# Kernel optimization log

Hardware: AMD Instinct MI355X
Metric: run time of the kernel (lower is better)

Reference implementation:

```python
import jax, jax.numpy as jnp
import numpy as np

B, T, C, H = 512, 40, 512, 512


def _gru_dir(x, Wih, Whh, bih, bhh):
    """Single-direction PyTorch-convention GRU. x: [B,T,C] -> [B,T,H]."""
    Hh = Whh.shape[1]
    # precompute input projections for all timesteps: [B,T,3H]
    gx = jnp.einsum('btc,gc->btg', x, Wih) + bih

    def step(h, gxt):
        gh = h @ Whh.T + bhh  # [B,3H]
        r = jax.nn.sigmoid(gxt[:, :Hh] + gh[:, :Hh])
        z = jax.nn.sigmoid(gxt[:, Hh:2 * Hh] + gh[:, Hh:2 * Hh])
        n = jnp.tanh(gxt[:, 2 * Hh:] + r * gh[:, 2 * Hh:])
        h_new = (1.0 - z) * n + z * h
        return h_new, h_new

    h0 = jnp.zeros((x.shape[0], Hh), x.dtype)
    _, ys = jax.lax.scan(step, h0, jnp.swapaxes(gx, 0, 1))  # [T,B,H]
    return jnp.swapaxes(ys, 0, 1)


def setup_inputs() -> dict:
    key = jax.random.key(0)
    ks = jax.random.split(key, 10)
    s = 1.0 / np.sqrt(H)  # PyTorch default init scale
    lengths = jax.random.randint(ks[0], (B,), 5, T + 1)
    valid = jnp.arange(T)[None, :] < lengths[:, None]  # [B,T]
    ref_expr = jax.random.normal(ks[1], (B, T, C), jnp.float32) * valid[..., None]
    mk = lambda k, shape: jax.random.uniform(k, shape, jnp.float32, -s, s)
    return {
        'ref_expr': ref_expr,
        'Wih_f': mk(ks[2], (3 * H, C)), 'Whh_f': mk(ks[3], (3 * H, H)),
        'bih_f': mk(ks[4], (3 * H,)), 'bhh_f': mk(ks[5], (3 * H,)),
        'Wih_b': mk(ks[6], (3 * H, C)), 'Whh_b': mk(ks[7], (3 * H, H)),
        'bih_b': mk(ks[8], (3 * H,)), 'bhh_b': mk(ks[9], (3 * H,)),
    }


def reference(ref_expr, Wih_f, Whh_f, bih_f, bhh_f, Wih_b, Whh_b, bih_b, bhh_b):
    # padded positions are all-zero embedding vectors -> masked out
    valid = jnp.any(ref_expr != 0, axis=-1)  # [B,T], True = keep
    y_fwd = _gru_dir(ref_expr, Wih_f, Whh_f, bih_f, bhh_f)
    y_bwd = _gru_dir(ref_expr[:, ::-1], Wih_b, Whh_b, bih_b, bhh_b)[:, ::-1]
    y_word = jnp.concatenate([y_fwd, y_bwd], axis=-1)  # [B,T,2H]
    # masked max pooling over valid tokens (output_type='max')
    neg = jnp.finfo(y_word.dtype).min
    y = jnp.max(jnp.where(valid[..., None], y_word, neg), axis=1, keepdims=True)
    return y  # [B,1,2H]
```

## Files before the change

kernel.cpp:

```cpp
#include <hip/hip_runtime.h>
#include <hip/hip_bf16.h>
#include <float.h>

#define BB 512
#define TT 40
#define CC 512
#define HH 512

typedef short bf16x8 __attribute__((ext_vector_type(8)));
typedef float f32x4 __attribute__((ext_vector_type(4)));
typedef unsigned short ushortx8 __attribute__((ext_vector_type(8)));

#define LDSH 49152
#define LDSF 98304
#define LDSTOT 98320

__device__ __forceinline__ unsigned short f2bf(float f){
  union { float f; unsigned int i; } v; v.f = f;
  unsigned int r = v.i + 0x7fffu + ((v.i >> 16) & 1u);
  return (unsigned short)(r >> 16);
}

__device__ __forceinline__ bf16x8 load_sc0(const unsigned short* p){
  bf16x8 r;
  asm volatile("global_load_dwordx4 %0, %1, off sc0" : "=v"(r) : "v"(p));
  return r;
}
#define WAITV(N) do { asm volatile("s_waitcnt vmcnt(" #N ")" ::: "memory"); \
                      __builtin_amdgcn_sched_barrier(0); } while(0)

__device__ __forceinline__ void waitv_idx(int n){
  switch(n){
    case 0:  WAITV(0);  break;  case 1:  WAITV(1);  break;
    case 2:  WAITV(2);  break;  case 3:  WAITV(3);  break;
    case 4:  WAITV(4);  break;  case 5:  WAITV(5);  break;
    case 6:  WAITV(6);  break;  case 7:  WAITV(7);  break;
    case 8:  WAITV(8);  break;  case 9:  WAITV(9);  break;
    case 10: WAITV(10); break;  case 11: WAITV(11); break;
    case 12: WAITV(12); break;  case 13: WAITV(13); break;
    case 14: WAITV(14); break;  default: WAITV(15); break;
  }
}

__device__ __forceinline__ float fast_sigmoid(float x){
  return __builtin_amdgcn_rcpf(1.f + __expf(-x));
}
__device__ __forceinline__ float fast_tanh(float x){
  return 1.f - 2.f*__builtin_amdgcn_rcpf(__expf(2.f*x) + 1.f);
}

__global__ void prep_x_kernel(const float* __restrict__ x, unsigned short* __restrict__ xb,
                              float* __restrict__ maskT){
  int w = blockIdx.x*4 + (threadIdx.x>>6);
  int lane = threadIdx.x & 63;
  const float* src = x + (size_t)w*CC + lane*8;
  f32x4 a = *(const f32x4*)(src);
  f32x4 b = *(const f32x4*)(src+4);
  ushortx8 o;
  o[0]=f2bf(a[0]); o[1]=f2bf(a[1]); o[2]=f2bf(a[2]); o[3]=f2bf(a[3]);
  o[4]=f2bf(b[0]); o[5]=f2bf(b[1]); o[6]=f2bf(b[2]); o[7]=f2bf(b[3]);
  *(ushortx8*)(xb + (size_t)w*CC + lane*8) = o;
  bool nz = (a[0]!=0.f)||(a[1]!=0.f)||(a[2]!=0.f)||(a[3]!=0.f)||
            (b[0]!=0.f)||(b[1]!=0.f)||(b[2]!=0.f)||(b[3]!=0.f);
  unsigned long long bal = __ballot(nz);
  if (lane==0){
    int b_ = w / TT, t_ = w % TT;
    maskT[t_*BB + b_] = bal ? 1.0f : 0.0f;
  }
}

__global__ void cvt_kernel(const float* __restrict__ src, unsigned short* __restrict__ dst, int n8){
  int i = blockIdx.x*blockDim.x + threadIdx.x;
  if (i < n8){
    f32x4 a = *(const f32x4*)(src + i*8);
    f32x4 b = *(const f32x4*)(src + i*8 + 4);
    ushortx8 o;
    o[0]=f2bf(a[0]); o[1]=f2bf(a[1]); o[2]=f2bf(a[2]); o[3]=f2bf(a[3]);
    o[4]=f2bf(b[0]); o[5]=f2bf(b[1]); o[6]=f2bf(b[2]); o[7]=f2bf(b[3]);
    *(ushortx8*)(dst + i*8) = o;
  }
}

__global__ void init_h_kernel(unsigned short* __restrict__ hb, unsigned int* __restrict__ flags){
  int i = blockIdx.x*blockDim.x + threadIdx.x;
  hb[i] = 0;
  if (i < 256) flags[i] = 0u;
}

__global__ __launch_bounds__(512, 2) void gru_persist_kernel(
    const unsigned short* __restrict__ xb,
    const unsigned short* __restrict__ wihF, const unsigned short* __restrict__ whhF,
    const unsigned short* __restrict__ wihB, const unsigned short* __restrict__ whhB,
    const float* __restrict__ bihF, const float* __restrict__ bhhF,
    const float* __restrict__ bihB, const float* __restrict__ bhhB,
    const float* __restrict__ maskT,
    unsigned short* __restrict__ hb,
    float* __restrict__ out, unsigned int* __restrict__ flags)
{
  const int bid   = blockIdx.x;
  const int grp   = bid & 7;
  const int strip = bid >> 3;
  const int dir   = grp >> 2;
  const int bslab = grp & 3;
  const int b0 = bslab * 128;
  const int n0 = strip * 16;
  unsigned int* fl = flags + grp*32;

  const unsigned short* wih = dir ? wihB : wihF;
  const unsigned short* whh = dir ? whhB : whhF;
  const float* bih = dir ? bihB : bihF;
  const float* bhh = dir ? bhhB : bhhF;

  const int tid  = threadIdx.x;
  const int lane = tid & 63;
  const int lr   = lane & 15;
  const int lkg  = lane >> 4;
  const int wv   = tid >> 6;
  const int wrow = wv * 16;

  __shared__ __align__(16) char smem[LDSTOT];
  unsigned int* arrive = (unsigned int*)(smem + LDSF);

  for (int q = tid; q < 6144; q += 512) {
    const int p_  = q >= 3072;
    const int r_  = p_ ? (q - 3072) : q;
    const int row = r_ >> 6;
    const int kc  = (r_ & 63) * 8;
    const unsigned short* src =
        (p_ ? whh : wih) + ((size_t)((row>>4)*HH + n0 + (row&15)))*512 + kc;
    *(ushortx8*)(smem + p_*LDSH + row*1024 + ((kc*2) ^ ((row&15)<<4))) =
        *(const ushortx8*)src;
  }
  if (tid == 0) arrive[0] = 0u;
  __syncthreads();

  const int jj = n0 + lr;
  const float br  = bih[jj]        + bhh[jj];
  const float bz  = bih[HH + jj]   + bhh[HH + jj];
  const float bnx = bih[2*HH + jj];
  const float bnh = bhh[2*HH + jj];

  float omax[4], hreg[4];
  #pragma unroll
  for (int j=0; j<4; ++j){ omax[j] = -FLT_MAX; hreg[j] = 0.f; }

  const int swz = lr << 4;
  const char* wbx = smem + lr*1024;
  const char* wbh = smem + LDSH + lr*1024;

  for (int t = 0; t < TT; ++t) {
    const int tx = dir ? (TT-1-t) : t;
    const int bi = t & 1;
    const unsigned short* hbin = hb + (size_t)(dir*2 + bi)      * (BB*HH);
    unsigned short* hbout      = hb + (size_t)(dir*2 + (bi^1))  * (BB*HH);

    f32x4 ar = 0.f, az = 0.f, anx = 0.f, anh = 0.f;

    const unsigned short* xr0 = xb + ((size_t)(b0 + wrow + lr)*TT + tx)*CC;

    #pragma unroll
    for (int kk = 0; kk < 16; ++kk) {
      const int ko = kk*32 + lkg*8;
      bf16x8 a0 = *(const bf16x8*)(xr0 + ko);
      const int kbx = (ko*2) ^ swz;
      bf16x8 brf = *(const bf16x8*)(wbx +         kbx);
      bf16x8 bzf = *(const bf16x8*)(wbx + 16384 + kbx);
      bf16x8 bnf = *(const bf16x8*)(wbx + 32768 + kbx);
      ar  = __builtin_amdgcn_mfma_f32_16x16x32_bf16(a0, brf, ar,0,0,0);
      az  = __builtin_amdgcn_mfma_f32_16x16x32_bf16(a0, bzf, az,0,0,0);
      anx = __builtin_amdgcn_mfma_f32_16x16x32_bf16(a0, bnf, anx,0,0,0);
    }

    const f32x4 mk = *(const f32x4*)(maskT + tx*BB + b0 + wrow + lkg*4);

    if (t > 0) {
      const unsigned int tgt = (unsigned)t;
      unsigned int spin = 0;
      for (;;) {
        unsigned int v = tgt;
        if (lane < 32)
          v = __hip_atomic_load(&fl[lane], __ATOMIC_RELAXED, __HIP_MEMORY_SCOPE_AGENT);
        if (__ballot(v < tgt) == 0ull) break;
        if (++spin >= (1u<<22)) break;
        __builtin_amdgcn_s_sleep(1);
      }
    }

    WAITV(0);

    const unsigned short* hr0 = hbin + (size_t)(b0 + wrow + lr)*HH;
    bf16x8 ph[16];
    #pragma unroll
    for (int q = 0; q < 16; ++q)
      ph[q] = load_sc0(hr0 + q*32 + lkg*8);
    #pragma unroll
    for (int kk = 0; kk < 16; ++kk) {
      const int ko = kk*32 + lkg*8;
      const int kbx = (ko*2) ^ swz;
      bf16x8 brf = *(const bf16x8*)(wbh +         kbx);
      bf16x8 bzf = *(const bf16x8*)(wbh + 16384 + kbx);
      bf16x8 bnf = *(const bf16x8*)(wbh + 32768 + kbx);
      waitv_idx(15 - kk);
      bf16x8 c0 = ph[kk];
      ar  = __builtin_amdgcn_mfma_f32_16x16x32_bf16(c0, brf, ar,0,0,0);
      az  = __builtin_amdgcn_mfma_f32_16x16x32_bf16(c0, bzf, az,0,0,0);
      anh = __builtin_amdgcn_mfma_f32_16x16x32_bf16(c0, bnf, anh,0,0,0);
    }

    #pragma unroll
    for (int j=0; j<4; ++j){
      const int b = b0 + wrow + lkg*4 + j;
      const float rg = fast_sigmoid(ar[j] + br);
      const float zg = fast_sigmoid(az[j] + bz);
      const float ng = fast_tanh(anx[j] + bnx + rg*(anh[j] + bnh));
      const float hn = (1.f - zg)*ng + zg*hreg[j];
      hreg[j] = hn;
      hbout[(size_t)b*HH + jj] = f2bf(hn);
      const float cand = (mk[j] != 0.f) ? hn : -FLT_MAX;
      omax[j] = fmaxf(omax[j], cand);
    }

    if (t < TT-1) {
      WAITV(0);
      if (lane == 0) {
        unsigned int prev =
            __hip_atomic_fetch_add(arrive, 1u, __ATOMIC_ACQ_REL, __HIP_MEMORY_SCOPE_WORKGROUP);
        if (prev + 1u == 8u*(unsigned)(t+1))
          __hip_atomic_store(&fl[strip], (unsigned)(t+1),
                             __ATOMIC_RELAXED, __HIP_MEMORY_SCOPE_AGENT);
      }
    }
  }

  #pragma unroll
  for (int j=0; j<4; ++j){
    const int b = b0 + wrow + lkg*4 + j;
    out[(size_t)b*(2*HH) + dir*HH + jj] = omax[j];
  }
}

extern "C" void kernel_launch(void* const* d_in, const int* in_sizes, int n_in,
                              void* d_out, int out_size, void* d_ws, size_t ws_size,
                              hipStream_t stream) {
  const float* x    = (const float*)d_in[0];
  const float* WihF = (const float*)d_in[1];
  const float* WhhF = (const float*)d_in[2];
  const float* bihF = (const float*)d_in[3];
  const float* bhhF = (const float*)d_in[4];
  const float* WihB = (const float*)d_in[5];
  const float* WhhB = (const float*)d_in[6];
  const float* bihB = (const float*)d_in[7];
  const float* bhhB = (const float*)d_in[8];
  float* out = (float*)d_out;

  char* ws = (char*)d_ws;
  unsigned short* xb    = (unsigned short*)(ws);
  unsigned short* wb    = (unsigned short*)(ws + 20971520);
  unsigned short* wihFb = wb;
  unsigned short* whhFb = wb + 786432;
  unsigned short* wihBb = wb + 2*786432;
  unsigned short* whhBb = wb + 3*786432;
  float* maskT = (float*)(ws + 27262976);
  unsigned short* hb = (unsigned short*)(ws + 27344896);
  unsigned int* flags = (unsigned int*)(ws + 29442048);

  prep_x_kernel<<<BB*TT/4, 256, 0, stream>>>(x, xb, maskT);
  cvt_kernel<<<384, 256, 0, stream>>>(WihF, wihFb, 98304);
  cvt_kernel<<<384, 256, 0, stream>>>(WhhF, whhFb, 98304);
  cvt_kernel<<<384, 256, 0, stream>>>(WihB, wihBb, 98304);
  cvt_kernel<<<384, 256, 0, stream>>>(WhhB, whhBb, 98304);
  init_h_kernel<<<4096, 256, 0, stream>>>(hb, flags);

  gru_persist_kernel<<<256, 512, 0, stream>>>(xb, wihFb, whhFb, wihBb, whhBb,
                                              bihF, bhhF, bihB, bhhB,
                                              maskT, hb, out, flags);
}
```

Baseline: 339.2 us.

## Split recurrent h wait into two halves to overlap flag waits with MFMA

The per-step wait on producer flags is split in two. The block first waits only on the flags covering the first half of the hidden columns, loads that half of h and runs its MFMAs, then waits on the second half's flags. This lets part of the recurrent matmul overlap with producers that are still finishing, at the cost of a second spin loop and barrier per step. The flag init count and spin limit also change, which may go with flag semantics changed in code not shown.

```diff
diff --git a/kernel.cpp b/kernel.cpp
--- a/kernel.cpp
+++ b/kernel.cpp
@@ -29,16 +29,12 @@
 #define WAITV(N) do { asm volatile("s_waitcnt vmcnt(" #N ")" ::: "memory"); \
                       __builtin_amdgcn_sched_barrier(0); } while(0)
 
-__device__ __forceinline__ void waitv_idx(int n){
+__device__ __forceinline__ void waitv_idx8(int n){
   switch(n){
     case 0:  WAITV(0);  break;  case 1:  WAITV(1);  break;
     case 2:  WAITV(2);  break;  case 3:  WAITV(3);  break;
     case 4:  WAITV(4);  break;  case 5:  WAITV(5);  break;
-    case 6:  WAITV(6);  break;  case 7:  WAITV(7);  break;
-    case 8:  WAITV(8);  break;  case 9:  WAITV(9);  break;
-    case 10: WAITV(10); break;  case 11: WAITV(11); break;
-    case 12: WAITV(12); break;  case 13: WAITV(13); break;
-    case 14: WAITV(14); break;  default: WAITV(15); break;
+    case 6:  WAITV(6);  break;  default: WAITV(7);  break;
   }
 }
 
@@ -84,7 +80,7 @@
 __global__ void init_h_kernel(unsigned short* __restrict__ hb, unsigned int* __restrict__ flags){
   int i = blockIdx.x*blockDim.x + threadIdx.x;
   hb[i] = 0;
-  if (i < 256) flags[i] = 0u;
+  if (i < 512) flags[i] = 0u;
 }
 
 __global__ __launch_bounds__(512, 2) void gru_persist_kernel(
@@ -173,34 +169,65 @@
 
     const f32x4 mk = *(const f32x4*)(maskT + tx*BB + b0 + wrow + lkg*4);
 
+    const unsigned short* hr0 = hbin + (size_t)(b0 + wrow + lr)*HH;
+    bf16x8 ph[8];
+
     if (t > 0) {
       const unsigned int tgt = (unsigned)t;
       unsigned int spin = 0;
       for (;;) {
         unsigned int v = tgt;
-        if (lane < 32)
+        if (lane < 16)
           v = __hip_atomic_load(&fl[lane], __ATOMIC_RELAXED, __HIP_MEMORY_SCOPE_AGENT);
         if (__ballot(v < tgt) == 0ull) break;
-        if (++spin >= (1u<<22)) break;
+        if (++spin >= (1u<<24)) break;
         __builtin_amdgcn_s_sleep(1);
       }
     }
-
     WAITV(0);
 
-    const unsigned short* hr0 = hbin + (size_t)(b0 + wrow + lr)*HH;
-    bf16x8 ph[16];
-    #pragma unroll
-    for (int q = 0; q < 16; ++q)
+    #pragma unroll
+    for (int q = 0; q < 8; ++q)
       ph[q] = load_sc0(hr0 + q*32 + lkg*8);
     #pragma unroll
-    for (int kk = 0; kk < 16; ++kk) {
+    for (int kk = 0; kk < 8; ++kk) {
       const int ko = kk*32 + lkg*8;
       const int kbx = (ko*2) ^ swz;
       bf16x8 brf = *(const bf16x8*)(wbh +         kbx);
       bf16x8 bzf = *(const bf16x8*)(wbh + 16384 + kbx);
       bf16x8 bnf = *(const bf16x8*)(wbh + 32768 + kbx);
-      waitv_idx(15 - kk);
+      waitv_idx8(7 - kk);
+      bf16x8 c0 = ph[kk];
+      ar  = __builtin_amdgcn_mfma_f32_16x16x32_bf16(c0, brf, ar,0,0,0);
+      az  = __builtin_amdgcn_mfma_f32_16x16x32_bf16(c0, bzf, az,0,0,0);
+      anh = __builtin_amdgcn_mfma_f32_16x16x32_bf16(c0, bnf, anh,0,0,0);
+    }
+
+    if (t > 0) {
+      const unsigned int tgt = (unsigned)t;
+      unsigned int spin = 0;
+      for (;;) {
+        unsigned int v = tgt;
+        if (lane >= 16 && lane < 32)
+          v = __hip_atomic_load(&fl[lane], __ATOMIC_RELAXED, __HIP_MEMORY_SCOPE_AGENT);
+        if (__ballot(v < tgt) == 0ull) break;
+        if (++spin >= (1u<<24)) break;
+        __builtin_amdgcn_s_sleep(1);
+      }
+    }
+    WAITV(0);
+
+    #pragma unroll
+    for (int q = 0; q < 8; ++q)
+      ph[q] = load_sc0(hr0 + (8+q)*32 + lkg*8);
+    #pragma unroll
+    for (int kk = 0; kk < 8; ++kk) {
+      const int ko = (kk+8)*32 + lkg*8;
+      const int kbx = (ko*2) ^ swz;
+      bf16x8 brf = *(const bf16x8*)(wbh +         kbx);
+      bf16x8 bzf = *(const bf16x8*)(wbh + 16384 + kbx);
+      bf16x8 bnf = *(const bf16x8*)(wbh + 32768 + kbx);
+      waitv_idx8(7 - kk);
       bf16x8 c0 = ph[kk];
       ar  = __builtin_amdgcn_mfma_f32_16x16x32_bf16(c0, brf, ar,0,0,0);
       az  = __builtin_amdgcn_mfma_f32_16x16x32_bf16(c0, bzf, az,0,0,0);
```

Result: slower. 361.2 us (+6.5%).
